# Performance work log

Measured on AMD Instinct MI355X. Metric: run time of the kernel, lower is better.

## Reference

```python
import jax, jax.numpy as jnp
import numpy as np

B, T, D, D_OUT = 8, 2048, 1024, 1024


def setup_inputs() -> dict:
    key = jax.random.key(0)
    k1, k2 = jax.random.split(key)
    x = jax.random.normal(k1, (B, T, D), dtype=jnp.float32)
    # dense projection params (Linear(D, D_OUT)); scaled init for stability
    W = jax.random.normal(k2, (D, D_OUT), dtype=jnp.float32) / np.sqrt(D)
    b = jnp.zeros((D_OUT,), dtype=jnp.float32)
    return {"x": x, "W": W, "b": b}


def reference(x, W, b):
    # x_: [B, T, D_OUT] projected tensor (self.dense(x))
    x_ = jnp.einsum("btd,de->bte", x, W) + b
    # correlation_matrix: [B, T, T], scaled by sqrt(d_out)
    scores = jnp.einsum("bte,bse->bts", x_, x_) / jnp.sqrt(jnp.asarray(D_OUT, x.dtype))
    # additive causal mask: -inf above the diagonal (triu, diagonal=1)
    causal = jnp.triu(jnp.full((T, T), -jnp.inf, dtype=x.dtype), k=1)
    scores = scores + causal
    # NOTE: original uses nn.Softmax(1) -> softmax over dim 1 (columns), not -1
    attn = jax.nn.softmax(scores, axis=1)
    # V is the RAW input x, not the projected x_
    return jnp.einsum("bts,bsd->btd", attn, x)
```

## Files before the change

kernel.cpp:

```cpp
#include <hip/hip_runtime.h>
#include <hip/hip_bf16.h>


#define B_ 8
#define T_ 2048
#define D_ 1024
#define E_ 1024
#define PIT 56
#define NCH 8
#define CHR (T_ / NCH)

typedef unsigned short u16;
typedef __attribute__((ext_vector_type(8))) short short8;
typedef __attribute__((ext_vector_type(4))) float floatx4;

__device__ __forceinline__ float b2f(u16 u) {
    unsigned v = ((unsigned)u) << 16;
    float f; __builtin_memcpy(&f, &v, 4); return f;
}
__device__ __forceinline__ u16 f2b(float f) {
    unsigned v; __builtin_memcpy(&v, &f, 4);
    v = (v + 0x7FFFu + ((v >> 16) & 1u)) >> 16;
    return (u16)v;
}
__device__ __forceinline__ unsigned pkbf(float a, float b) {
    __hip_bfloat162 h = __float22bfloat162_rn(make_float2(a, b));
    unsigned u; __builtin_memcpy(&u, &h, 4); return u;
}

__device__ __forceinline__ void gl2lds16(const u16* gp, u16* lp) {
    __builtin_amdgcn_global_load_lds(
        (const __attribute__((address_space(1))) void*)(gp),
        (__attribute__((address_space(3))) void*)(lp), 16, 0, 0);
}

__device__ __forceinline__ void stage8(const u16* src, size_t srow, int kc,
                                       u16* lds, int wid, int lane)
{
    const int rl = lane >> 3, c = lane & 7;
    const int g = ((c ^ rl) << 3);
#pragma unroll
    for (int cc = 0; cc < 2; cc++) {
        const int r = cc * 64 + wid * 8;
        gl2lds16(src + (size_t)(r + rl) * srow + kc + g, &lds[r * 64]);
    }
}

__device__ __forceinline__ void gemm_step(const u16* As_, const u16* Bs_,
                                          int wr, int wc, int l15, int q, int sw,
                                          floatx4 (&acc)[2][4])
{
#pragma unroll
    for (int h = 0; h < 2; h++) {
        short8 a[2], b2[4];
#pragma unroll
        for (int i = 0; i < 2; i++)
            a[i] = *(const short8*)&As_[(wr + i * 16 + l15) * 64 + (((h * 4 + q) ^ sw) << 3)];
#pragma unroll
        for (int j = 0; j < 4; j++)
            b2[j] = *(const short8*)&Bs_[(wc + j * 16 + l15) * 64 + (((h * 4 + q) ^ sw) << 3)];
#pragma unroll
        for (int i = 0; i < 2; i++)
#pragma unroll
            for (int j = 0; j < 4; j++)
                acc[i][j] = __builtin_amdgcn_mfma_f32_16x16x32_bf16(a[i], b2[j], acc[i][j], 0, 0, 0);
    }
}

__device__ __forceinline__ float* mr_ptr(u16* S, int which, int b, int s) {
    const int row = which * 32 + b * 4 + (s >> 9);
    return (float*)(S + (size_t)row * T_ + 1024 + (s & 511) * 2);
}
__device__ __forceinline__ float* part_ptr(u16* S, int which, int c, int b, int s) {
    const int row = 64 + which * 256 + (c * 8 + b) * 4 + (s >> 9);
    return (float*)(S + (size_t)row * T_ + 1024 + (s & 511) * 2);
}

__global__ __launch_bounds__(256) void k0_wt(const float* __restrict__ W,
                                             u16* __restrict__ WT)
{
    __shared__ float Ws[64 * 68];
    const int tid = threadIdx.x;
    const int k0 = blockIdx.x * 64, n0 = blockIdx.y * 64;
#pragma unroll
    for (int u = 0; u < 4; u++) {
        const int c = tid + 256 * u;
        const int row = c >> 4, c4 = c & 15;
        float4 v = *(const float4*)(W + (size_t)(k0 + row) * E_ + n0 + c4 * 4);
        *(float4*)&Ws[row * 68 + c4 * 4] = v;
    }
    __syncthreads();
#pragma unroll
    for (int u = 0; u < 2; u++) {
        const int c = tid + 256 * u;
        const int n = c >> 3, kc = c & 7;
        unsigned pk[4];
#pragma unroll
        for (int j = 0; j < 4; j++)
            pk[j] = pkbf(Ws[(kc * 8 + 2 * j) * 68 + n], Ws[(kc * 8 + 2 * j + 1) * 68 + n]);
        *(uint4*)(WT + (size_t)(n0 + n) * D_ + k0 + kc * 8) = make_uint4(pk[0], pk[1], pk[2], pk[3]);
    }
}

__global__ __launch_bounds__(256) void k00_xt(const float* __restrict__ x,
                                              u16* __restrict__ XT,
                                              u16* __restrict__ xbf,
                                              int do_xt)
{
    __shared__ float Xs[64 * 68];
    const int tid = threadIdx.x;
    const int s0 = blockIdx.x * 64, d0 = blockIdx.y * 64, b = blockIdx.z;
    const float* xb = x + (size_t)b * T_ * D_;
#pragma unroll
    for (int u = 0; u < 4; u++) {
        const int c = tid + 256 * u;
        const int row = c >> 4, c4 = c & 15;
        float4 v = *(const float4*)(xb + (size_t)(s0 + row) * D_ + d0 + c4 * 4);
        *(float4*)&Xs[row * 68 + c4 * 4] = v;
    }
    __syncthreads();
#pragma unroll
    for (int u = 0; u < 2; u++) {
        const int c = tid + 256 * u;
        const int row = c >> 3, off = c & 7;
        unsigned pk[4];
#pragma unroll
        for (int j = 0; j < 4; j++)
            pk[j] = pkbf(Xs[row * 68 + off * 8 + 2 * j], Xs[row * 68 + off * 8 + 2 * j + 1]);
        *(uint4*)(xbf + ((size_t)(b * T_ + s0 + row)) * D_ + d0 + off * 8) =
            make_uint4(pk[0], pk[1], pk[2], pk[3]);
    }
    if (!do_xt) return;
#pragma unroll
    for (int u = 0; u < 2; u++) {
        const int c = tid + 256 * u;
        const int d = c >> 3, sc = c & 7;
        unsigned pk[4];
#pragma unroll
        for (int j = 0; j < 4; j++)
            pk[j] = pkbf(Xs[(sc * 8 + 2 * j) * 68 + d], Xs[(sc * 8 + 2 * j + 1) * 68 + d]);
        *(uint4*)(XT + ((size_t)(b * D_ + d0 + d)) * T_ + s0 + sc * 8) =
            make_uint4(pk[0], pk[1], pk[2], pk[3]);
    }
}

__global__ __launch_bounds__(512, 4) void k1_proj(const u16* __restrict__ xbf,
                                                  const u16* __restrict__ WT,
                                                  const float* __restrict__ bias,
                                                  u16* __restrict__ y)
{
    __shared__ u16 As[2][128 * 64];
    __shared__ u16 Bs[2][128 * 64];
    const int tid = threadIdx.x;
    const int lane = tid & 63, wid = tid >> 6;
    const int wr = (wid >> 1) * 32, wc = (wid & 1) * 64;
    const int l15 = lane & 15, q = lane >> 4;
    const int sw = l15 & 7;
    const int lin = blockIdx.y * 8 + blockIdx.x;
    const int v = (lin & 7) * 128 + (lin >> 3);
    const int n0 = (v & 7) * 128, m0 = (v >> 3) * 128;
    const u16* Ab = xbf + (size_t)m0 * D_;
    const u16* Bb = WT + (size_t)n0 * D_;

    floatx4 acc[2][4];
#pragma unroll
    for (int i = 0; i < 2; i++)
#pragma unroll
        for (int j = 0; j < 4; j++) acc[i][j] = (floatx4){0.f, 0.f, 0.f, 0.f};

    stage8(Ab, D_, 0, As[0], wid, lane);
    stage8(Bb, D_, 0, Bs[0], wid, lane);
    __syncthreads();
    int cur = 0;
    for (int t = 0; t < 16; t++) {
        if (t + 1 < 16) {
            stage8(Ab, D_, (t + 1) * 64, As[cur ^ 1], wid, lane);
            stage8(Bb, D_, (t + 1) * 64, Bs[cur ^ 1], wid, lane);
        }
        gemm_step(As[cur], Bs[cur], wr, wc, l15, q, sw, acc);
        __syncthreads();
        cur ^= 1;
    }
    float bv[4];
#pragma unroll
    for (int j = 0; j < 4; j++) bv[j] = bias[n0 + wc + j * 16 + l15];
#pragma unroll
    for (int i = 0; i < 2; i++)
#pragma unroll
        for (int j = 0; j < 4; j++)
#pragma unroll
            for (int r = 0; r < 4; r++) {
                const int gm = m0 + wr + i * 16 + q * 4 + r;
                const int gn = n0 + wc + j * 16 + l15;
                y[(size_t)gm * E_ + gn] = f2b(acc[i][j][r] + bv[j]);
            }
}

__global__ __launch_bounds__(512, 4) void k2_score(const u16* __restrict__ y,
                                                   u16* __restrict__ S)
{
    __shared__ u16 As[2][128 * 64];
    __shared__ u16 Bs[2][128 * 64];
    const int tid = threadIdx.x;
    const int lane = tid & 63, wid = tid >> 6;
    const int wr = (wid >> 1) * 32, wc = (wid & 1) * 64;
    const int l15 = lane & 15, q = lane >> 4;
    const int sw = l15 & 7;
    const int lin = blockIdx.x;
    const int b = lin & 7;
    int idx = lin >> 3;
    int it = 0, base = 0;
    while (base + it + 1 <= idx) { base += it + 1; it++; }
    const int js = idx - base;
    const int t0 = it * 128, s0 = js * 128;
    const u16* yb = y + (size_t)b * T_ * E_;
    const u16* Ab = yb + (size_t)t0 * E_;
    const u16* Bb = yb + (size_t)s0 * E_;

    floatx4 acc[2][4];
#pragma unroll
    for (int i = 0; i < 2; i++)
#pragma unroll
        for (int j = 0; j < 4; j++) acc[i][j] = (floatx4){0.f, 0.f, 0.f, 0.f};

    stage8(Ab, E_, 0, As[0], wid, lane);
    stage8(Bb, E_, 0, Bs[0], wid, lane);
    __syncthreads();
    int cur = 0;
    for (int t = 0; t < 16; t++) {
        if (t + 1 < 16) {
            stage8(Ab, E_, (t + 1) * 64, As[cur ^ 1], wid, lane);
            stage8(Bb, E_, (t + 1) * 64, Bs[cur ^ 1], wid, lane);
        }
        gemm_step(As[cur], Bs[cur], wr, wc, l15, q, sw, acc);
        __syncthreads();
        cur ^= 1;
    }
#pragma unroll
    for (int i = 0; i < 2; i++)
#pragma unroll
        for (int j = 0; j < 4; j++)
#pragma unroll
            for (int r = 0; r < 4; r++) {
                const int t = t0 + wr + i * 16 + q * 4 + r;
                const int s = s0 + wc + j * 16 + l15;
                u16 o = (t < s) ? (u16)0xFF7F : f2b(acc[i][j][r] * 0.03125f);
                S[((size_t)(b * T_ + t)) * T_ + s] = o;
            }
}

__global__ __launch_bounds__(256) void k2b_part(u16* __restrict__ S)
{
    __shared__ u16 St[CHR * 64];
    __shared__ float sm[4][64], sz[4][64];
    const int tid = threadIdx.x;
    const int lane = tid & 63, w = tid >> 6;
    const int s0 = blockIdx.x * 64;
    const int c  = blockIdx.y;
    const int b  = blockIdx.z;
    const int tb = max(c * CHR, s0);
    const int te = (c + 1) * CHR;
    if (tb >= te) return;
    const int R = te - tb;
    const u16* Sb = S + (size_t)b * T_ * T_;
    for (int r0 = 0; r0 < R; r0 += 32) {
        const int row = r0 + (tid >> 3), off = tid & 7;
        *(uint4*)&St[row * 64 + off * 8] =
            *(const uint4*)(Sb + (size_t)(tb + row) * T_ + s0 + off * 8);
    }
    __syncthreads();
    const int rb = w * 64;
    float m4[4] = {-3e38f, -3e38f, -3e38f, -3e38f};
    float z4[4] = {0.f, 0.f, 0.f, 0.f};
    float mt = -3e38f;
    if (rb < R) {
#pragma unroll 4
        for (int i = 0; i < 64; i += 4)
#pragma unroll
            for (int j = 0; j < 4; j++)
                m4[j] = fmaxf(m4[j], b2f(St[(rb + i + j) * 64 + lane]));
        mt = fmaxf(fmaxf(m4[0], m4[1]), fmaxf(m4[2], m4[3]));
#pragma unroll 4
        for (int i = 0; i < 64; i += 4)
#pragma unroll
            for (int j = 0; j < 4; j++)
                z4[j] += __expf(b2f(St[(rb + i + j) * 64 + lane]) - mt);
    }
    sm[w][lane] = mt;
    sz[w][lane] = (z4[0] + z4[1]) + (z4[2] + z4[3]);
    __syncthreads();
    if (tid < 64) {
        float mm = sm[0][tid];
#pragma unroll
        for (int rr = 1; rr < 4; rr++) mm = fmaxf(mm, sm[rr][tid]);
        float zz = 0.f;
#pragma unroll
        for (int rr = 0; rr < 4; rr++) zz += sz[rr][tid] * __expf(sm[rr][tid] - mm);
        *part_ptr(S, 0, c, b, s0 + tid) = mm;
        *part_ptr(S, 1, c, b, s0 + tid) = zz;
    }
}

__global__ __launch_bounds__(256) void k2c_comb(u16* __restrict__ S)
{
    const int s = blockIdx.x * 256 + threadIdx.x;
    const int b = blockIdx.y;
    float M = -3e38f, Z = 0.f;
    for (int c = s >> 8; c < NCH; c++) {
        const float mc = *part_ptr(S, 0, c, b, s);
        const float zc = *part_ptr(S, 1, c, b, s);
        if (mc > M) { Z = Z * __expf(M - mc) + zc; M = mc; }
        else        { Z += zc * __expf(mc - M); }
    }
    *mr_ptr(S, 0, b, s) = M;
    *mr_ptr(S, 1, b, s) = 1.0f / Z;
}

__global__ __launch_bounds__(256) void k3_pnorm(u16* __restrict__ S)
{
    const int row = blockIdx.x;
    const int b = row >> 11;
    const int t = row & (T_ - 1);
    const int sEnd = ((t >> 7) + 1) << 7;
    const int s0 = threadIdx.x * 8;
    if (s0 >= sEnd) return;
    u16* Sp = S + (size_t)row * T_ + s0;
    const float* mp = mr_ptr(S, 0, b, s0);
    const float* rp = mr_ptr(S, 1, b, s0);
    float mv[8], rv[8];
    *(float4*)&mv[0] = *(const float4*)mp;
    *(float4*)&mv[4] = *((const float4*)mp + 1);
    *(float4*)&rv[0] = *(const float4*)rp;
    *(float4*)&rv[4] = *((const float4*)rp + 1);
    ushort4 v0 = *(ushort4*)Sp;
    ushort4 v1 = *(ushort4*)(Sp + 4);
    u16 vv[8] = { v0.x, v0.y, v0.z, v0.w, v1.x, v1.y, v1.z, v1.w };
    u16 ov[8];
#pragma unroll
    for (int i = 0; i < 8; i++) {
        const int s = s0 + i;
        float p = 0.f;
        if (s <= t) p = __expf(b2f(vv[i]) - mv[i]) * rv[i];
        ov[i] = f2b(p);
    }
    *(ushort4*)Sp       = make_ushort4(ov[0], ov[1], ov[2], ov[3]);
    *(ushort4*)(Sp + 4) = make_ushort4(ov[4], ov[5], ov[6], ov[7]);
}

__global__ __launch_bounds__(512, 4) void k4_fast(const u16* __restrict__ P,
                                                  const u16* __restrict__ XT,
                                                  float* __restrict__ out)
{
    __shared__ u16 As[2][128 * 64];
    __shared__ u16 Bs[2][128 * 64];
    const int tid = threadIdx.x;
    const int lane = tid & 63, wid = tid >> 6;
    const int wr = (wid >> 1) * 32, wc = (wid & 1) * 64;
    const int l15 = lane & 15, q = lane >> 4;
    const int sw = l15 & 7;
    const int lin = blockIdx.x;
    const int b = lin & 7;
    const int r8 = lin >> 3;
    const int d0 = (r8 & 7) * 128;
    const int it = (T_ / 128 - 1) - (r8 >> 3);
    const int t0 = it * 128;
    const u16* Pb = P + (size_t)b * T_ * T_ + (size_t)t0 * T_;
    const u16* Xb = XT + (size_t)(b * D_ + d0) * T_;

    floatx4 acc[2][4];
#pragma unroll
    for (int i = 0; i < 2; i++)
#pragma unroll
        for (int j = 0; j < 4; j++) acc[i][j] = (floatx4){0.f, 0.f, 0.f, 0.f};

    const int nt = (it + 1) * 2;
    stage8(Pb, T_, 0, As[0], wid, lane);
    stage8(Xb, T_, 0, Bs[0], wid, lane);
    __syncthreads();
    int cur = 0;
    for (int t = 0; t < nt; t++) {
        if (t + 1 < nt) {
            stage8(Pb, T_, (t + 1) * 64, As[cur ^ 1], wid, lane);
            stage8(Xb, T_, (t + 1) * 64, Bs[cur ^ 1], wid, lane);
        }
        gemm_step(As[cur], Bs[cur], wr, wc, l15, q, sw, acc);
        __syncthreads();
        cur ^= 1;
    }
#pragma unroll
    for (int i = 0; i < 2; i++)
#pragma unroll
        for (int j = 0; j < 4; j++)
#pragma unroll
            for (int r = 0; r < 4; r++) {
                const int gt = t0 + wr + i * 16 + q * 4 + r;
                const int gd = d0 + wc + j * 16 + l15;
                out[(size_t)(b * T_ + gt) * D_ + gd] = acc[i][j][r];
            }
}

__global__ __launch_bounds__(256) void k4_fb(const u16* __restrict__ P,
                                             const float* __restrict__ x,
                                             float* __restrict__ out)
{
    __shared__ u16 As[128 * PIT];
    __shared__ u16 Bs[128 * PIT];
    const int tid = threadIdx.x;
    const int lane = tid & 63, wid = tid >> 6;
    const int wr = (wid >> 1) * 64, wc = (wid & 1) * 64;
    const int l15 = lane & 15, q = lane >> 4;
    const int it = (T_ / 128 - 1) - blockIdx.y;
    const int t0 = it * 128;
    const int d0 = blockIdx.x * 128;
    const int b = blockIdx.z;
    const u16* Pb = P + (size_t)b * T_ * T_;
    const float* xb = x + (size_t)b * T_ * D_;
    const int gn = tid & 127;
    const int kh0 = (tid >> 7) * 2;

    floatx4 acc[4][4];
#pragma unroll
    for (int i = 0; i < 4; i++)
#pragma unroll
        for (int j = 0; j < 4; j++) acc[i][j] = (floatx4){0.f, 0.f, 0.f, 0.f};

    const int kend = t0 + 128;
    for (int k0 = 0; k0 < kend; k0 += 32) {
        __syncthreads();
#pragma unroll
        for (int u = 0; u < 2; u++) {
            const int c = tid * 2 + u;
            const int row = c >> 2, off = c & 3;
            *(uint4*)&As[row * PIT + off * 8] =
                *(const uint4*)(Pb + (size_t)(t0 + row) * T_ + k0 + off * 8);
        }
#pragma unroll
        for (int u = 0; u < 2; u++) {
            const int kh = kh0 + u;
            float f[8];
#pragma unroll
            for (int j = 0; j < 8; j++)
                f[j] = xb[(size_t)(k0 + kh * 8 + j) * D_ + d0 + gn];
            uint4 pk = make_uint4(pkbf(f[0], f[1]), pkbf(f[2], f[3]),
                                  pkbf(f[4], f[5]), pkbf(f[6], f[7]));
            *(uint4*)&Bs[gn * PIT + kh * 8] = pk;
        }
        __syncthreads();
        short8 a[4], b2[4];
#pragma unroll
        for (int i = 0; i < 4; i++) a[i] = *(const short8*)&As[(wr + i * 16 + l15) * PIT + q * 8];
#pragma unroll
        for (int j = 0; j < 4; j++) b2[j] = *(const short8*)&Bs[(wc + j * 16 + l15) * PIT + q * 8];
#pragma unroll
        for (int i = 0; i < 4; i++)
#pragma unroll
            for (int j = 0; j < 4; j++)
                acc[i][j] = __builtin_amdgcn_mfma_f32_16x16x32_bf16(a[i], b2[j], acc[i][j], 0, 0, 0);
    }
#pragma unroll
    for (int i = 0; i < 4; i++)
#pragma unroll
        for (int j = 0; j < 4; j++)
#pragma unroll
            for (int r = 0; r < 4; r++) {
                const int gt = t0 + wr + i * 16 + q * 4 + r;
                const int gd = d0 + wc + j * 16 + l15;
                out[(size_t)(b * T_ + gt) * D_ + gd] = acc[i][j][r];
            }
}

extern "C" void kernel_launch(void* const* d_in, const int* in_sizes, int n_in,
                              void* d_out, int out_size, void* d_ws, size_t ws_size,
                              hipStream_t stream)
{
    const float* x    = (const float*)d_in[0];
    const float* W    = (const float*)d_in[1];
    const float* bias = (const float*)d_in[2];
    float* outf = (float*)d_out;
    u16*   y    = (u16*)d_out;
    u16*   WT   = y + ((size_t)1 << 24);
    u16*   S    = (u16*)d_ws;
    u16*   xbf  = S;
    u16*   XT   = S + ((size_t)1 << 25);
    const bool fast = ws_size >= ((size_t)96 << 20);

    dim3 g0(D_ / 64, E_ / 64);
    k0_wt<<<g0, 256, 0, stream>>>(W, WT);

    dim3 g00(T_ / 64, D_ / 64, B_);
    k00_xt<<<g00, 256, 0, stream>>>(x, XT, xbf, fast ? 1 : 0);

    dim3 g1(E_ / 128, (B_ * T_) / 128);
    k1_proj<<<g1, 512, 0, stream>>>(xbf, WT, bias, y);

    dim3 g2(136 * B_);
    k2_score<<<g2, 512, 0, stream>>>(y, S);

    dim3 gp(T_ / 64, NCH, B_);
    k2b_part<<<gp, 256, 0, stream>>>(S);

    dim3 gc(T_ / 256, B_);
    k2c_comb<<<gc, 256, 0, stream>>>(S);

    dim3 g3(B_ * T_);
    k3_pnorm<<<g3, 256, 0, stream>>>(S);

    dim3 g4((D_ / 128) * (T_ / 128) * B_);
    if (fast) k4_fast<<<g4, 512, 0, stream>>>(S, XT, outf);
    else {
        dim3 g4b(D_ / 128, T_ / 128, B_);
        k4_fb<<<g4b, 256, 0, stream>>>(S, x, outf);
    }
}
```

Baseline: 294.3 us.

## Halve GEMM K-tile to 32 and double occupancy in proj, score and PV kernels

Shrinks the K step of the three bf16 MFMA GEMM kernels from 64 to 32. The smaller step halves LDS per block, and launch bounds rise to 8 blocks per CU so more waves can hide latency. Staging and the XOR swizzle are rewritten for 32-wide rows, with one 16-byte async load per lane per operand. In exchange each kernel runs twice as many loop iterations and barriers, and the swizzle over 4 chunks may cause more LDS bank conflicts.

```diff
diff --git a/kernel.cpp b/kernel.cpp
--- a/kernel.cpp
+++ b/kernel.cpp
@@ -34,37 +34,31 @@
         (__attribute__((address_space(3))) void*)(lp), 16, 0, 0);
 }
 
-__device__ __forceinline__ void stage8(const u16* src, size_t srow, int kc,
-                                       u16* lds, int wid, int lane)
-{
-    const int rl = lane >> 3, c = lane & 7;
-    const int g = ((c ^ rl) << 3);
-#pragma unroll
-    for (int cc = 0; cc < 2; cc++) {
-        const int r = cc * 64 + wid * 8;
-        gl2lds16(src + (size_t)(r + rl) * srow + kc + g, &lds[r * 64]);
-    }
-}
-
-__device__ __forceinline__ void gemm_step(const u16* As_, const u16* Bs_,
-                                          int wr, int wc, int l15, int q, int sw,
-                                          floatx4 (&acc)[2][4])
-{
-#pragma unroll
-    for (int h = 0; h < 2; h++) {
-        short8 a[2], b2[4];
-#pragma unroll
-        for (int i = 0; i < 2; i++)
-            a[i] = *(const short8*)&As_[(wr + i * 16 + l15) * 64 + (((h * 4 + q) ^ sw) << 3)];
-#pragma unroll
-        for (int j = 0; j < 4; j++)
-            b2[j] = *(const short8*)&Bs_[(wc + j * 16 + l15) * 64 + (((h * 4 + q) ^ sw) << 3)];
-#pragma unroll
-        for (int i = 0; i < 2; i++)
-#pragma unroll
-            for (int j = 0; j < 4; j++)
-                acc[i][j] = __builtin_amdgcn_mfma_f32_16x16x32_bf16(a[i], b2[j], acc[i][j], 0, 0, 0);
-    }
+__device__ __forceinline__ void stage32(const u16* src, size_t srow, int kc,
+                                        u16* lds, int wid, int lane)
+{
+    const int rl = lane >> 2, c = lane & 3;
+    const int g = ((c ^ (rl & 3)) << 3);
+    gl2lds16(src + (size_t)(wid * 16 + rl) * srow + kc + g, &lds[wid * 16 * 32]);
+}
+
+__device__ __forceinline__ void gemm_step32(const u16* As_, const u16* Bs_,
+                                            int wr, int wc, int l15, int q,
+                                            floatx4 (&acc)[2][4])
+{
+    const int sx = (q ^ (l15 & 3)) << 3;
+    short8 a[2], b2[4];
+#pragma unroll
+    for (int i = 0; i < 2; i++)
+        a[i] = *(const short8*)&As_[(wr + i * 16 + l15) * 32 + sx];
+#pragma unroll
+    for (int j = 0; j < 4; j++)
+        b2[j] = *(const short8*)&Bs_[(wc + j * 16 + l15) * 32 + sx];
+#pragma unroll
+    for (int i = 0; i < 2; i++)
+#pragma unroll
+        for (int j = 0; j < 4; j++)
+            acc[i][j] = __builtin_amdgcn_mfma_f32_16x16x32_bf16(a[i], b2[j], acc[i][j], 0, 0, 0);
 }
 
 __device__ __forceinline__ float* mr_ptr(u16* S, int which, int b, int s) {
@@ -144,18 +138,17 @@
     }
 }
 
-__global__ __launch_bounds__(512, 4) void k1_proj(const u16* __restrict__ xbf,
+__global__ __launch_bounds__(512, 8) void k1_proj(const u16* __restrict__ xbf,
                                                   const u16* __restrict__ WT,
                                                   const float* __restrict__ bias,
                                                   u16* __restrict__ y)
 {
-    __shared__ u16 As[2][128 * 64];
-    __shared__ u16 Bs[2][128 * 64];
+    __shared__ u16 As[2][128 * 32];
+    __shared__ u16 Bs[2][128 * 32];
     const int tid = threadIdx.x;
     const int lane = tid & 63, wid = tid >> 6;
     const int wr = (wid >> 1) * 32, wc = (wid & 1) * 64;
     const int l15 = lane & 15, q = lane >> 4;
-    const int sw = l15 & 7;
     const int lin = blockIdx.y * 8 + blockIdx.x;
     const int v = (lin & 7) * 128 + (lin >> 3);
     const int n0 = (v & 7) * 128, m0 = (v >> 3) * 128;
@@ -168,16 +161,16 @@
 #pragma unroll
         for (int j = 0; j < 4; j++) acc[i][j] = (floatx4){0.f, 0.f, 0.f, 0.f};
 
-    stage8(Ab, D_, 0, As[0], wid, lane);
-    stage8(Bb, D_, 0, Bs[0], wid, lane);
+    stage32(Ab, D_, 0, As[0], wid, lane);
+    stage32(Bb, D_, 0, Bs[0], wid, lane);
     __syncthreads();
     int cur = 0;
-    for (int t = 0; t < 16; t++) {
-        if (t + 1 < 16) {
-            stage8(Ab, D_, (t + 1) * 64, As[cur ^ 1], wid, lane);
-            stage8(Bb, D_, (t + 1) * 64, Bs[cur ^ 1], wid, lane);
+    for (int t = 0; t < 32; t++) {
+        if (t + 1 < 32) {
+            stage32(Ab, D_, (t + 1) * 32, As[cur ^ 1], wid, lane);
+            stage32(Bb, D_, (t + 1) * 32, Bs[cur ^ 1], wid, lane);
         }
-        gemm_step(As[cur], Bs[cur], wr, wc, l15, q, sw, acc);
+        gemm_step32(As[cur], Bs[cur], wr, wc, l15, q, acc);
         __syncthreads();
         cur ^= 1;
     }
@@ -196,16 +189,15 @@
             }
 }
 
-__global__ __launch_bounds__(512, 4) void k2_score(const u16* __restrict__ y,
+__global__ __launch_bounds__(512, 8) void k2_score(const u16* __restrict__ y,
                                                    u16* __restrict__ S)
 {
-    __shared__ u16 As[2][128 * 64];
-    __shared__ u16 Bs[2][128 * 64];
+    __shared__ u16 As[2][128 * 32];
+    __shared__ u16 Bs[2][128 * 32];
     const int tid = threadIdx.x;
     const int lane = tid & 63, wid = tid >> 6;
     const int wr = (wid >> 1) * 32, wc = (wid & 1) * 64;
     const int l15 = lane & 15, q = lane >> 4;
-    const int sw = l15 & 7;
     const int lin = blockIdx.x;
     const int b = lin & 7;
     int idx = lin >> 3;
@@ -223,16 +215,16 @@
 #pragma unroll
         for (int j = 0; j < 4; j++) acc[i][j] = (floatx4){0.f, 0.f, 0.f, 0.f};
 
-    stage8(Ab, E_, 0, As[0], wid, lane);
-    stage8(Bb, E_, 0, Bs[0], wid, lane);
+    stage32(Ab, E_, 0, As[0], wid, lane);
+    stage32(Bb, E_, 0, Bs[0], wid, lane);
     __syncthreads();
     int cur = 0;
-    for (int t = 0; t < 16; t++) {
-        if (t + 1 < 16) {
-            stage8(Ab, E_, (t + 1) * 64, As[cur ^ 1], wid, lane);
-            stage8(Bb, E_, (t + 1) * 64, Bs[cur ^ 1], wid, lane);
+    for (int t = 0; t < 32; t++) {
+        if (t + 1 < 32) {
+            stage32(Ab, E_, (t + 1) * 32, As[cur ^ 1], wid, lane);
+            stage32(Bb, E_, (t + 1) * 32, Bs[cur ^ 1], wid, lane);
         }
-        gemm_step(As[cur], Bs[cur], wr, wc, l15, q, sw, acc);
+        gemm_step32(As[cur], Bs[cur], wr, wc, l15, q, acc);
         __syncthreads();
         cur ^= 1;
     }
@@ -347,17 +339,16 @@
     *(ushort4*)(Sp + 4) = make_ushort4(ov[4], ov[5], ov[6], ov[7]);
 }
 
-__global__ __launch_bounds__(512, 4) void k4_fast(const u16* __restrict__ P,
+__global__ __launch_bounds__(512, 8) void k4_fast(const u16* __restrict__ P,
                                                   const u16* __restrict__ XT,
                                                   float* __restrict__ out)
 {
-    __shared__ u16 As[2][128 * 64];
-    __shared__ u16 Bs[2][128 * 64];
+    __shared__ u16 As[2][128 * 32];
+    __shared__ u16 Bs[2][128 * 32];
     const int tid = threadIdx.x;
     const int lane = tid & 63, wid = tid >> 6;
     const int wr = (wid >> 1) * 32, wc = (wid & 1) * 64;
     const int l15 = lane & 15, q = lane >> 4;
-    const int sw = l15 & 7;
     const int lin = blockIdx.x;
     const int b = lin & 7;
     const int r8 = lin >> 3;
@@ -373,17 +364,17 @@
 #pragma unroll
         for (int j = 0; j < 4; j++) acc[i][j] = (floatx4){0.f, 0.f, 0.f, 0.f};
 
-    const int nt = (it + 1) * 2;
-    stage8(Pb, T_, 0, As[0], wid, lane);
-    stage8(Xb, T_, 0, Bs[0], wid, lane);
+    const int nt = (it + 1) * 4;
+    stage32(Pb, T_, 0, As[0], wid, lane);
+    stage32(Xb, T_, 0, Bs[0], wid, lane);
     __syncthreads();
     int cur = 0;
     for (int t = 0; t < nt; t++) {
         if (t + 1 < nt) {
-            stage8(Pb, T_, (t + 1) * 64, As[cur ^ 1], wid, lane);
-            stage8(Xb, T_, (t + 1) * 64, Bs[cur ^ 1], wid, lane);
+            stage32(Pb, T_, (t + 1) * 32, As[cur ^ 1], wid, lane);
+            stage32(Xb, T_, (t + 1) * 32, Bs[cur ^ 1], wid, lane);
         }
-        gemm_step(As[cur], Bs[cur], wr, wc, l15, q, sw, acc);
+        gemm_step32(As[cur], Bs[cur], wr, wc, l15, q, acc);
         __syncthreads();
         cur ^= 1;
     }
```

After: 335.9 us. 1.14x slower.
